# Kernel optimization log

Hardware: AMD Instinct MI355X
Metric: run time of the kernel (lower is better)

## Reference

```python
import jax, jax.numpy as jnp
import numpy as np

S, B, T, D = 25, 64, 640, 128
NUM_CHANNELS = 4
T_WAV = 1.0 / 16000.0
LOG_F_MEAN = 5.02654
LOG_F_STD = 0.373288


def _i_2pi():
    # harmonic index per output dim: dims grouped as num_freq blocks of num_channels
    i = jnp.floor_divide(jnp.arange(D), NUM_CHANNELS) + 1  # [D]
    return i.astype(jnp.float32) * (2.0 * np.pi)


def _k_T():
    return jnp.arange(T, dtype=jnp.float32) * T_WAV  # [T]


def setup_inputs() -> dict:
    key = jax.random.key(0)
    k1, k2, k3, k4, k5 = jax.random.split(key, 5)
    x = jax.random.normal(k1, (S, B, 1, T), dtype=jnp.float32)
    nlf = jax.random.normal(k2, (S, B, 1, 1), dtype=jnp.float32)
    tau = jax.random.uniform(k3, (S, B, 1, 1), dtype=jnp.float32)
    a = 0.1 + 0.1 * jax.random.normal(k4, (D,), dtype=jnp.float32)
    phi = jax.random.normal(k5, (D,), dtype=jnp.float32)
    return {"x": x, "nlf": nlf, "tau": tau, "a": a, "phi": phi}


def reference(x, nlf, tau, a, phi):
    i_2pi = _i_2pi()          # [D]
    k_T = _k_T()              # [T]
    f = jnp.exp(nlf[..., 0, 0] * LOG_F_STD + LOG_F_MEAN)   # [S,B]
    t = k_T[None, None, :] - tau[..., 0, :]                  # [S,B,T]
    f_t = f[..., None] * t                                   # [S,B,T]
    # deg: [S,B,T,D] = f_t outer i_2pi + phi ; sin basis
    deg = f_t[..., None] * i_2pi[None, None, None, :] + phi
    s = jnp.sin(deg)                                         # [S,B,T,D]
    x_SBT = x[:, :, 0, :]                                    # [S,B,T]
    sin_x = jnp.einsum('sbtd,sbt->sbd', s, x_SBT)            # [S,B,D]
    h = a * sin_x                                            # [S,B,D]
    return h
```

## Files before the change

kernel.cpp:

```cpp
#include <hip/hip_runtime.h>
#include <math.h>


#define S_DIM 25
#define B_DIM 64
#define T_DIM 640
#define D_DIM 128
#define NCHUNK 8
#define CLEN (T_DIM / NCHUNK)

__global__ __launch_bounds__(256) void sinenet_kernel(
    const float* __restrict__ x,
    const float* __restrict__ nlf,
    const float* __restrict__ tau,
    const float* __restrict__ a,
    const float* __restrict__ phi,
    float* __restrict__ out)
{
    __shared__ float lds_x[T_DIM];
    __shared__ float red[2][NCHUNK][32];
    __shared__ float fin[64];

    const int bid   = blockIdx.x;
    const int tid   = threadIdx.x;
    const int lane  = tid & 63;
    const int wid   = tid >> 6;
    const int h     = lane & 31;
    const int chunk = wid * 2 + (lane >> 5);
    const int t0    = chunk * CLEN;

    if (tid < T_DIM / 4)
        reinterpret_cast<float4*>(lds_x)[tid] =
            reinterpret_cast<const float4*>(x + (size_t)bid * T_DIM)[tid];

    const float tau_v = tau[bid];
    const float f     = expf(nlf[bid] * 0.373288f + 5.02654f);
    const float i_f   = (float)(h + 1);
    const float T_WAV = 1.0f / 16000.0f;

    const float dr0 = i_f * (f * T_WAV);
    const float dr  = dr0 - floorf(dr0);
    const float sD  = __builtin_amdgcn_sinf(dr);
    const float cD  = __builtin_amdgcn_cosf(dr);

    const float c1 = cD,                        s1 = sD;
    const float c2 = fmaf(c1, cD, -(s1 * sD)),  s2 = fmaf(s1, cD, c1 * sD);
    const float c3 = fmaf(c2, cD, -(s2 * sD)),  s3 = fmaf(s2, cD, c2 * sD);
    const float c4 = fmaf(c3, cD, -(s3 * sD)),  s4 = fmaf(s3, cD, c3 * sD);
    const float c5 = fmaf(c4, cD, -(s4 * sD)),  s5 = fmaf(s4, cD, c4 * sD);
    const float c6 = fmaf(c5, cD, -(s5 * sD)),  s6 = fmaf(s5, cD, c5 * sD);
    const float c7 = fmaf(c6, cD, -(s6 * sD)),  s7 = fmaf(s6, cD, c6 * sD);
    const float c8 = fmaf(c7, cD, -(s7 * sD)),  s8 = fmaf(s7, cD, c7 * sD);

    const float tv0 = (float)t0 * T_WAV - tau_v;
    const float ft0 = f * tv0;
    const float u0  = ft0 - floorf(ft0);
    const float p0  = i_f * u0;
    const float w0  = p0 - floorf(p0);
    float s = __builtin_amdgcn_sinf(w0);
    float c = __builtin_amdgcn_cosf(w0);

    __syncthreads();

    float acc_s = 0.0f, acc_c = 0.0f;
    const float4* __restrict__ xp4 = reinterpret_cast<const float4*>(&lds_x[t0]);
    #pragma unroll
    for (int m = 0; m < CLEN / 8; ++m) {
        const float4 xa = xp4[2 * m];
        const float4 xb = xp4[2 * m + 1];

        float P = xa.x;
        P = fmaf(xa.y, c1, P); P = fmaf(xa.z, c2, P); P = fmaf(xa.w, c3, P);
        P = fmaf(xb.x, c4, P); P = fmaf(xb.y, c5, P); P = fmaf(xb.z, c6, P);
        P = fmaf(xb.w, c7, P);

        float Q = xa.y * s1;
        Q = fmaf(xa.z, s2, Q); Q = fmaf(xa.w, s3, Q); Q = fmaf(xb.x, s4, Q);
        Q = fmaf(xb.y, s5, Q); Q = fmaf(xb.z, s6, Q); Q = fmaf(xb.w, s7, Q);

        acc_s = fmaf(s, P, acc_s); acc_s = fmaf(c, Q, acc_s);
        acc_c = fmaf(c, P, acc_c); acc_c = fmaf(-s, Q, acc_c);

        const float sn = fmaf(s, c8, c * s8);
        const float cn = fmaf(c, c8, -(s * s8));
        s = sn; c = cn;
    }

    red[0][chunk][h] = acc_s;
    red[1][chunk][h] = acc_c;
    __syncthreads();

    if (tid < 64) {
        const int part = tid >> 5, hh = tid & 31;
        float v = 0.0f;
        #pragma unroll
        for (int cc = 0; cc < NCHUNK; ++cc)
            v += red[part][cc][hh];
        fin[tid] = v;
    }
    __syncthreads();

    if (tid < D_DIM) {
        const int   i0 = tid >> 2;
        const float Ss = fin[i0];
        const float Cs = fin[32 + i0];
        float pr = phi[tid] * 0.15915494309189535f;
        pr = pr - floorf(pr);
        const float sp = __builtin_amdgcn_sinf(pr);
        const float cp = __builtin_amdgcn_cosf(pr);
        out[(size_t)bid * D_DIM + tid] = a[tid] * fmaf(cp, Ss, sp * Cs);
    }
}

extern "C" void kernel_launch(void* const* d_in, const int* in_sizes, int n_in,
                              void* d_out, int out_size, void* d_ws, size_t ws_size,
                              hipStream_t stream) {
    const float* x   = (const float*)d_in[0];
    const float* nlf = (const float*)d_in[1];
    const float* tau = (const float*)d_in[2];
    const float* a   = (const float*)d_in[3];
    const float* phi = (const float*)d_in[4];
    float* out = (float*)d_out;

    const int n_sb = S_DIM * B_DIM;
    sinenet_kernel<<<n_sb, 256, 0, stream>>>(x, nlf, tau, a, phi, out);
}
```

Measured before the change: 9.474 us.

## Read x directly from global, pack sin/cos math as float2, merge final reduction

Each thread now reads its chunk of x straight from global memory as float4 instead of staging it in LDS, which removes the LDS copy and one barrier. The per-harmonic P/Q and the s/c accumulator updates are rewritten as float2 operations so the compiler can emit packed FMA instructions. The final two reduction stages are merged: 64 threads each sum one harmonic's partials and write two output dims with vectorized phi/a loads and a float2 store, dropping another barrier. exp is rewritten as exp2 with a folded fma. The trade-off is redundant global reads of x across the 32 harmonic lanes, which rely on the cache instead of LDS.

```diff
diff --git a/kernel.cpp b/kernel.cpp
--- a/kernel.cpp
+++ b/kernel.cpp
@@ -9,6 +9,13 @@
 #define NCHUNK 8
 #define CLEN (T_DIM / NCHUNK)
 
+__device__ __forceinline__ float2 f2fma(float s, float2 b, float2 c) {
+    return make_float2(fmaf(s, b.x, c.x), fmaf(s, b.y, c.y));
+}
+__device__ __forceinline__ float2 f2scale(float2 a, float s) {
+    return make_float2(a.x * s, a.y * s);
+}
+
 __global__ __launch_bounds__(256) void sinenet_kernel(
     const float* __restrict__ x,
     const float* __restrict__ nlf,
@@ -17,9 +24,7 @@
     const float* __restrict__ phi,
     float* __restrict__ out)
 {
-    __shared__ float lds_x[T_DIM];
-    __shared__ float red[2][NCHUNK][32];
-    __shared__ float fin[64];
+    __shared__ float2 red[NCHUNK][32];
 
     const int bid   = blockIdx.x;
     const int tid   = threadIdx.x;
@@ -29,12 +34,8 @@
     const int chunk = wid * 2 + (lane >> 5);
     const int t0    = chunk * CLEN;
 
-    if (tid < T_DIM / 4)
-        reinterpret_cast<float4*>(lds_x)[tid] =
-            reinterpret_cast<const float4*>(x + (size_t)bid * T_DIM)[tid];
-
+    const float f     = exp2f(fmaf(nlf[bid], 0.53854075f, 7.2517643f));
     const float tau_v = tau[bid];
-    const float f     = expf(nlf[bid] * 0.373288f + 5.02654f);
     const float i_f   = (float)(h + 1);
     const float T_WAV = 1.0f / 16000.0f;
 
@@ -51,64 +52,65 @@
     const float c6 = fmaf(c5, cD, -(s5 * sD)),  s6 = fmaf(s5, cD, c5 * sD);
     const float c7 = fmaf(c6, cD, -(s6 * sD)),  s7 = fmaf(s6, cD, c6 * sD);
     const float c8 = fmaf(c7, cD, -(s7 * sD)),  s8 = fmaf(s7, cD, c7 * sD);
+    const float2 t1 = make_float2(c1, s1), t2 = make_float2(c2, s2);
+    const float2 t3 = make_float2(c3, s3), t4 = make_float2(c4, s4);
+    const float2 t5 = make_float2(c5, s5), t6 = make_float2(c6, s6);
+    const float2 t7 = make_float2(c7, s7);
 
     const float tv0 = (float)t0 * T_WAV - tau_v;
     const float ft0 = f * tv0;
     const float u0  = ft0 - floorf(ft0);
     const float p0  = i_f * u0;
     const float w0  = p0 - floorf(p0);
-    float s = __builtin_amdgcn_sinf(w0);
-    float c = __builtin_amdgcn_cosf(w0);
+    float2 u = make_float2(__builtin_amdgcn_sinf(w0), __builtin_amdgcn_cosf(w0));
+    float2 w = make_float2(u.y, -u.x);
 
-    __syncthreads();
-
-    float acc_s = 0.0f, acc_c = 0.0f;
-    const float4* __restrict__ xp4 = reinterpret_cast<const float4*>(&lds_x[t0]);
+    float2 A = make_float2(0.0f, 0.0f);
+    const float4* __restrict__ xp4 =
+        reinterpret_cast<const float4*>(x + (size_t)bid * T_DIM + t0);
     #pragma unroll
     for (int m = 0; m < CLEN / 8; ++m) {
         const float4 xa = xp4[2 * m];
         const float4 xb = xp4[2 * m + 1];
 
-        float P = xa.x;
-        P = fmaf(xa.y, c1, P); P = fmaf(xa.z, c2, P); P = fmaf(xa.w, c3, P);
-        P = fmaf(xb.x, c4, P); P = fmaf(xb.y, c5, P); P = fmaf(xb.z, c6, P);
-        P = fmaf(xb.w, c7, P);
+        float2 pq = make_float2(xa.x, 0.0f);
+        pq = f2fma(xa.y, t1, pq);
+        pq = f2fma(xa.z, t2, pq);
+        pq = f2fma(xa.w, t3, pq);
+        pq = f2fma(xb.x, t4, pq);
+        pq = f2fma(xb.y, t5, pq);
+        pq = f2fma(xb.z, t6, pq);
+        pq = f2fma(xb.w, t7, pq);
 
-        float Q = xa.y * s1;
-        Q = fmaf(xa.z, s2, Q); Q = fmaf(xa.w, s3, Q); Q = fmaf(xb.x, s4, Q);
-        Q = fmaf(xb.y, s5, Q); Q = fmaf(xb.z, s6, Q); Q = fmaf(xb.w, s7, Q);
+        A = f2fma(pq.x, u, A);
+        A = f2fma(pq.y, w, A);
 
-        acc_s = fmaf(s, P, acc_s); acc_s = fmaf(c, Q, acc_s);
-        acc_c = fmaf(c, P, acc_c); acc_c = fmaf(-s, Q, acc_c);
-
-        const float sn = fmaf(s, c8, c * s8);
-        const float cn = fmaf(c, c8, -(s * s8));
-        s = sn; c = cn;
+        const float2 un = f2fma( s8, w, f2scale(u, c8));
+        const float2 wn = f2fma(-s8, u, f2scale(w, c8));
+        u = un; w = wn;
     }
 
-    red[0][chunk][h] = acc_s;
-    red[1][chunk][h] = acc_c;
+    red[chunk][h] = A;
     __syncthreads();
 
     if (tid < 64) {
-        const int part = tid >> 5, hh = tid & 31;
-        float v = 0.0f;
+        const int hh = tid >> 1;
+        float2 v = red[0][hh];
         #pragma unroll
-        for (int cc = 0; cc < NCHUNK; ++cc)
-            v += red[part][cc][hh];
-        fin[tid] = v;
-    }
-    __syncthreads();
-
-    if (tid < D_DIM) {
-        const int   i0 = tid >> 2;
-        const float Ss = fin[i0];
-        const float Cs = fin[32 + i0];
-        float pr = phi[tid] * 0.15915494309189535f;
-        pr = pr - floorf(pr);
-        const float sp = __builtin_amdgcn_sinf(pr);
-        const float cp = __builtin_amdgcn_cosf(pr);
-        out[(size_t)bid * D_DIM + tid] = a[tid] * fmaf(cp, Ss, sp * Cs);
+        for (int cc = 1; cc < NCHUNK; ++cc) {
+            v.x += red[cc][hh].x;
+            v.y += red[cc][hh].y;
+        }
+        const float2 ph2 = reinterpret_cast<const float2*>(phi)[tid];
+        const float2 a2  = reinterpret_cast<const float2*>(a)[tid];
+        float pr0 = ph2.x * 0.15915494309189535f;  pr0 -= floorf(pr0);
+        float pr1 = ph2.y * 0.15915494309189535f;  pr1 -= floorf(pr1);
+        const float o0 = a2.x * fmaf(__builtin_amdgcn_cosf(pr0), v.x,
+                                     __builtin_amdgcn_sinf(pr0) * v.y);
+        const float o1 = a2.y * fmaf(__builtin_amdgcn_cosf(pr1), v.x,
+                                     __builtin_amdgcn_sinf(pr1) * v.y);
+        reinterpret_cast<float2*>(out + (size_t)bid * D_DIM)[tid] =
+            make_float2(o0, o1);
     }
 }
 
```

New measurement: 10.96 us. 15.7% more time.
